# Performance work log

Hardware: AMD Instinct MI355X
Metric: run time of the kernel (lower is better)

The kernel has to match this reference:

```python
import jax, jax.numpy as jnp
import numpy as np

K = 2  # top-k experts per token


def setup_inputs() -> dict:
    key = jax.random.key(0)
    k1, k2, k3, k4 = jax.random.split(key, 4)
    B, S, D, E = 4, 4096, 1024, 64
    x = jax.random.normal(k1, (B, S, D), dtype=jnp.float32)
    gate_w = jax.random.normal(k2, (E, D), dtype=jnp.float32) * (1.0 / np.sqrt(D))
    noise_weight = jax.random.normal(k3, (E,), dtype=jnp.float32) * 0.02
    noise = jax.random.normal(k4, (B, S, E), dtype=jnp.float32)  # randn_like(logits) * noisy_std(=1.0)
    return {"x": x, "gate_w": gate_w, "noise_weight": noise_weight, "noise": noise}


def reference(x, gate_w, noise_weight, noise):
    E = gate_w.shape[0]
    # logits = x @ W^T  -> [B, S, E]
    logits = jnp.einsum("bsd,ed->bse", x, gate_w)
    logits_noisy = logits + noise * noise_weight  # noisy_std = 1.0 folded into `noise`
    top_vals, top_idx = jax.lax.top_k(logits_noisy, K)  # [B,S,K]
    # scatter top-k logits into a -inf mask, then softmax over experts
    keep = jax.nn.one_hot(top_idx, E, dtype=jnp.bool_).any(axis=-2)  # [B,S,E]
    neg_inf = jnp.finfo(logits_noisy.dtype).min
    sparse = jnp.where(keep, logits_noisy, neg_inf)
    weights = jax.nn.softmax(sparse, axis=-1)
    return weights, top_idx
```

## Files before the change

### kernel.cpp

```cpp
#include <hip/hip_runtime.h>
#include <math.h>


#define DDIM 1024
#define NEXP 64
#define NTOK 16384
#define NSPLIT 4
#define CPB 4

typedef float f4 __attribute__((ext_vector_type(4)));
typedef short s8 __attribute__((ext_vector_type(8)));
typedef unsigned int u32;

static __device__ __forceinline__ void split3(float f, short& h, short& m, short& l) {
    const u32 uf = __float_as_uint(f);
    h = (short)(uf >> 16);
    const float r1 = f - __uint_as_float(uf & 0xffff0000u);
    const u32 u1 = __float_as_uint(r1);
    m = (short)(u1 >> 16);
    const float r2 = r1 - __uint_as_float(u1 & 0xffff0000u);
    l = (short)(__float_as_uint(r2) >> 16);
}

static __device__ __forceinline__ void gl_lds16(const void* g, void* l) {
    __builtin_amdgcn_global_load_lds(
        (const __attribute__((address_space(1))) u32*)g,
        (__attribute__((address_space(3))) u32*)l, 16, 0, 0);
}

__global__ __launch_bounds__(256)
void w_prep(const float* __restrict__ gw, short* __restrict__ wimg) {
    const int uid = blockIdx.x * 256 + threadIdx.x;
    const int c   = uid >> 9;
    const int kk  = (uid >> 8) & 1;
    const int e   = (uid >> 2) & 63;
    const int q   = uid & 3;
    const int k0  = c * 64 + kk * 32 + q * 8;
    const float* src = gw + (size_t)e * DDIM + k0;
    s8 hv, mv, lv;
    #pragma unroll
    for (int j = 0; j < 8; ++j) {
        short h, m, l;
        split3(src[j], h, m, l);
        hv[j] = h; mv[j] = m; lv[j] = l;
    }
    const size_t base = (size_t)c * 1536 + (kk * 3) * 256
                      + (e >> 4) * 64 + q * 16 + (e & 15);
    *(s8*)(wimg + (base      ) * 8) = hv;
    *(s8*)(wimg + (base + 256) * 8) = mv;
    *(s8*)(wimg + (base + 512) * 8) = lv;
}

__global__ __launch_bounds__(256, 4)
void gemm_partial(const float* __restrict__ x,
                  const short* __restrict__ wimg,
                  float* __restrict__ part)
{
    __shared__ short bs[1536 * 8];

    const int tid   = threadIdx.x;
    const int lane  = tid & 63;
    const int wv    = tid >> 6;
    const int m     = lane & 15;
    const int q     = lane >> 4;
    const int tile  = blockIdx.x & 255;
    const int split = blockIdx.x >> 8;
    const int tokBase = tile * 64 + wv * 16;

    const float* xrow = x + (size_t)(tokBase + m) * DDIM
                      + split * (CPB * 64) + q * 8;

    f4 acc0[4], acc1[4];
    #pragma unroll
    for (int t = 0; t < 4; ++t) { acc0[t] = (f4)0.f; acc1[t] = (f4)0.f; }

    f4 stage[2][4];
    stage[0][0] = *(const f4*)(xrow);
    stage[0][1] = *(const f4*)(xrow + 4);
    stage[0][2] = *(const f4*)(xrow + 32);
    stage[0][3] = *(const f4*)(xrow + 36);

    #pragma unroll
    for (int cc = 0; cc < CPB; ++cc) {
        const short* chunk = wimg + (size_t)(split * CPB + cc) * (1536 * 8);
        __syncthreads();
        #pragma unroll
        for (int i = 0; i < 6; ++i) {
            const int off = (wv * 6 + i) * 512;
            gl_lds16(chunk + off + lane * 8, &bs[off]);
        }
        __syncthreads();

        if (cc + 1 < CPB) {
            const float* s = xrow + (cc + 1) * 64;
            stage[(cc + 1) & 1][0] = *(const f4*)(s);
            stage[(cc + 1) & 1][1] = *(const f4*)(s + 4);
            stage[(cc + 1) & 1][2] = *(const f4*)(s + 32);
            stage[(cc + 1) & 1][3] = *(const f4*)(s + 36);
        }

        s8 ah[2], am[2], al[2];
        const float* sv = (const float*)stage[cc & 1];
        #pragma unroll
        for (int kk = 0; kk < 2; ++kk)
            #pragma unroll
            for (int j = 0; j < 8; ++j) {
                short h, mm, l;
                split3(sv[kk * 8 + j], h, mm, l);
                ah[kk][j] = h; am[kk][j] = mm; al[kk][j] = l;
            }

        #pragma unroll
        for (int kk = 0; kk < 2; ++kk) {
            #pragma unroll
            for (int t = 0; t < 4; ++t) {
                const int pb = (kk * 3) * 256 + t * 64 + lane;
                const s8 bh = *(const s8*)&bs[(pb      ) * 8];
                const s8 bm = *(const s8*)&bs[(pb + 256) * 8];
                const s8 bl = *(const s8*)&bs[(pb + 512) * 8];
                acc0[t] = __builtin_amdgcn_mfma_f32_16x16x32_bf16(ah[kk], bh, acc0[t], 0, 0, 0);
                acc1[t] = __builtin_amdgcn_mfma_f32_16x16x32_bf16(ah[kk], bm, acc1[t], 0, 0, 0);
                acc1[t] = __builtin_amdgcn_mfma_f32_16x16x32_bf16(am[kk], bh, acc1[t], 0, 0, 0);
                acc1[t] = __builtin_amdgcn_mfma_f32_16x16x32_bf16(ah[kk], bl, acc1[t], 0, 0, 0);
                acc1[t] = __builtin_amdgcn_mfma_f32_16x16x32_bf16(am[kk], bm, acc1[t], 0, 0, 0);
                acc1[t] = __builtin_amdgcn_mfma_f32_16x16x32_bf16(al[kk], bh, acc1[t], 0, 0, 0);
            }
        }
    }

    #pragma unroll
    for (int t = 0; t < 4; ++t)
        #pragma unroll
        for (int r = 0; r < 4; ++r)
            part[((size_t)split * NTOK + tokBase + q * 4 + r) * NEXP + m + 16 * t]
                = acc0[t][r] + acc1[t][r];
}

__global__ __launch_bounds__(256)
void reduce_topk(const float* __restrict__ part,
                 const float* __restrict__ noise_weight,
                 const float* __restrict__ noise,
                 float* __restrict__ out_w,
                 float* __restrict__ out_i)
{
    const int lane  = threadIdx.x & 63;
    const int wv    = threadIdx.x >> 6;
    const int token = blockIdx.x * 4 + wv;

    float sum = 0.f;
    #pragma unroll
    for (int s = 0; s < NSPLIT; ++s)
        sum += part[((size_t)s * NTOK + token) * NEXP + lane];

    const float ln = fmaf(noise[(size_t)token * NEXP + lane], noise_weight[lane], sum);

    float v1 = ln; int i1 = lane;
    #pragma unroll
    for (int off = 32; off > 0; off >>= 1) {
        const float vo = __shfl_xor(v1, off, 64);
        const int   io = __shfl_xor(i1, off, 64);
        if (vo > v1 || (vo == v1 && io < i1)) { v1 = vo; i1 = io; }
    }
    float v2 = (lane == i1) ? -3.4e38f : ln; int i2 = lane;
    #pragma unroll
    for (int off = 32; off > 0; off >>= 1) {
        const float vo = __shfl_xor(v2, off, 64);
        const int   io = __shfl_xor(i2, off, 64);
        if (vo > v2 || (vo == v2 && io < i2)) { v2 = vo; i2 = io; }
    }

    const float d   = expf(v2 - v1);
    const float inv = 1.f / (1.f + d);
    const float wgt = (lane == i1) ? inv : ((lane == i2) ? d * inv : 0.f);
    out_w[(size_t)token * NEXP + lane] = wgt;
    if (lane == 0) {
        out_i[(size_t)token * 2]     = (float)i1;
        out_i[(size_t)token * 2 + 1] = (float)i2;
    }
}

extern "C" void kernel_launch(void* const* d_in, const int* in_sizes, int n_in,
                              void* d_out, int out_size, void* d_ws, size_t ws_size,
                              hipStream_t stream) {
    const float* x     = (const float*)d_in[0];
    const float* gw    = (const float*)d_in[1];
    const float* nwt   = (const float*)d_in[2];
    const float* noise = (const float*)d_in[3];
    float* out_w = (float*)d_out;
    float* out_i = (float*)d_out + (size_t)NTOK * NEXP;

    short* wimg = (short*)d_ws;
    float* part = (float*)((char*)d_ws + 512 * 1024);

    hipLaunchKernelGGL(w_prep, dim3(32), dim3(256), 0, stream, gw, wimg);
    hipLaunchKernelGGL(gemm_partial, dim3(256 * NSPLIT), dim3(256), 0, stream,
                       x, wimg, part);
    hipLaunchKernelGGL(reduce_topk, dim3(NTOK / 4), dim3(256), 0, stream,
                       part, nwt, noise, out_w, out_i);
}
```

Before: 123.4 us.

## Fuse gating GEMM with top-k softmax, dropping split-K partials

Merges the split-K GEMM and the reduce/top-k kernel into one kernel. Each block handles 16 tokens over the full K dimension, with each wave owning 16 experts. Logits are staged in a small LDS tile, then the noisy top-2 softmax runs in place. This removes the partial-sum buffer round trip and one kernel launch. The trade-off is that each wave now reads B fragments directly from global memory instead of sharing LDS-staged weights, and each x row is loaded redundantly by all four waves.

```diff
diff --git a/kernel.cpp b/kernel.cpp
--- a/kernel.cpp
+++ b/kernel.cpp
@@ -5,8 +5,6 @@
 #define DDIM 1024
 #define NEXP 64
 #define NTOK 16384
-#define NSPLIT 4
-#define CPB 4
 
 typedef float f4 __attribute__((ext_vector_type(4)));
 typedef short s8 __attribute__((ext_vector_type(8)));
@@ -20,12 +18,6 @@
     m = (short)(u1 >> 16);
     const float r2 = r1 - __uint_as_float(u1 & 0xffff0000u);
     l = (short)(__float_as_uint(r2) >> 16);
-}
-
-static __device__ __forceinline__ void gl_lds16(const void* g, void* l) {
-    __builtin_amdgcn_global_load_lds(
-        (const __attribute__((address_space(1))) u32*)g,
-        (__attribute__((address_space(3))) u32*)l, 16, 0, 0);
 }
 
 __global__ __launch_bounds__(256)
@@ -51,131 +43,115 @@
     *(s8*)(wimg + (base + 512) * 8) = lv;
 }
 
-__global__ __launch_bounds__(256, 4)
-void gemm_partial(const float* __restrict__ x,
-                  const short* __restrict__ wimg,
-                  float* __restrict__ part)
+__global__ __launch_bounds__(256, 3)
+void gate_fused(const float* __restrict__ x,
+                const short* __restrict__ wimg,
+                const float* __restrict__ noise_weight,
+                const float* __restrict__ noise,
+                float* __restrict__ out_w,
+                float* __restrict__ out_i)
 {
-    __shared__ short bs[1536 * 8];
+    __shared__ float L[16][66];
 
-    const int tid   = threadIdx.x;
-    const int lane  = tid & 63;
-    const int wv    = tid >> 6;
-    const int m     = lane & 15;
-    const int q     = lane >> 4;
-    const int tile  = blockIdx.x & 255;
-    const int split = blockIdx.x >> 8;
-    const int tokBase = tile * 64 + wv * 16;
+    const int tid  = threadIdx.x;
+    const int lane = tid & 63;
+    const int wv   = tid >> 6;
+    const int m    = lane & 15;
+    const int q    = lane >> 4;
+    const int tokBase = blockIdx.x * 16;
 
-    const float* xrow = x + (size_t)(tokBase + m) * DDIM
-                      + split * (CPB * 64) + q * 8;
+    const float* xrow = x + (size_t)(tokBase + m) * DDIM + q * 8;
+    const short* wb   = wimg + ((size_t)wv * 64 + lane) * 8;
 
-    f4 acc0[4], acc1[4];
-    #pragma unroll
-    for (int t = 0; t < 4; ++t) { acc0[t] = (f4)0.f; acc1[t] = (f4)0.f; }
+    f4 acc0 = (f4)0.f, acc1 = (f4)0.f;
 
-    f4 stage[2][4];
-    stage[0][0] = *(const f4*)(xrow);
-    stage[0][1] = *(const f4*)(xrow + 4);
-    stage[0][2] = *(const f4*)(xrow + 32);
-    stage[0][3] = *(const f4*)(xrow + 36);
+    f4 sa[2][4];
+    sa[0][0] = *(const f4*)(xrow);
+    sa[0][1] = *(const f4*)(xrow + 4);
+    sa[0][2] = *(const f4*)(xrow + 32);
+    sa[0][3] = *(const f4*)(xrow + 36);
 
-    #pragma unroll
-    for (int cc = 0; cc < CPB; ++cc) {
-        const short* chunk = wimg + (size_t)(split * CPB + cc) * (1536 * 8);
-        __syncthreads();
-        #pragma unroll
-        for (int i = 0; i < 6; ++i) {
-            const int off = (wv * 6 + i) * 512;
-            gl_lds16(chunk + off + lane * 8, &bs[off]);
-        }
-        __syncthreads();
+    #pragma unroll 2
+    for (int cc = 0; cc < 16; ++cc) {
+        const int cur = cc & 1;
 
-        if (cc + 1 < CPB) {
+        const short* p = wb + (size_t)cc * (1536 * 8);
+        const s8 bh0 = *(const s8*)(p);
+        const s8 bm0 = *(const s8*)(p +  256 * 8);
+        const s8 bl0 = *(const s8*)(p +  512 * 8);
+        const s8 bh1 = *(const s8*)(p +  768 * 8);
+        const s8 bm1 = *(const s8*)(p + 1024 * 8);
+        const s8 bl1 = *(const s8*)(p + 1280 * 8);
+
+        if (cc + 1 < 16) {
             const float* s = xrow + (cc + 1) * 64;
-            stage[(cc + 1) & 1][0] = *(const f4*)(s);
-            stage[(cc + 1) & 1][1] = *(const f4*)(s + 4);
-            stage[(cc + 1) & 1][2] = *(const f4*)(s + 32);
-            stage[(cc + 1) & 1][3] = *(const f4*)(s + 36);
+            sa[cur ^ 1][0] = *(const f4*)(s);
+            sa[cur ^ 1][1] = *(const f4*)(s + 4);
+            sa[cur ^ 1][2] = *(const f4*)(s + 32);
+            sa[cur ^ 1][3] = *(const f4*)(s + 36);
         }
 
-        s8 ah[2], am[2], al[2];
-        const float* sv = (const float*)stage[cc & 1];
+        s8 ah[2], am_[2], al[2];
+        const float* sv = (const float*)sa[cur];
         #pragma unroll
         for (int kk = 0; kk < 2; ++kk)
             #pragma unroll
             for (int j = 0; j < 8; ++j) {
                 short h, mm, l;
                 split3(sv[kk * 8 + j], h, mm, l);
-                ah[kk][j] = h; am[kk][j] = mm; al[kk][j] = l;
+                ah[kk][j] = h; am_[kk][j] = mm; al[kk][j] = l;
             }
 
-        #pragma unroll
-        for (int kk = 0; kk < 2; ++kk) {
-            #pragma unroll
-            for (int t = 0; t < 4; ++t) {
-                const int pb = (kk * 3) * 256 + t * 64 + lane;
-                const s8 bh = *(const s8*)&bs[(pb      ) * 8];
-                const s8 bm = *(const s8*)&bs[(pb + 256) * 8];
-                const s8 bl = *(const s8*)&bs[(pb + 512) * 8];
-                acc0[t] = __builtin_amdgcn_mfma_f32_16x16x32_bf16(ah[kk], bh, acc0[t], 0, 0, 0);
-                acc1[t] = __builtin_amdgcn_mfma_f32_16x16x32_bf16(ah[kk], bm, acc1[t], 0, 0, 0);
-                acc1[t] = __builtin_amdgcn_mfma_f32_16x16x32_bf16(am[kk], bh, acc1[t], 0, 0, 0);
-                acc1[t] = __builtin_amdgcn_mfma_f32_16x16x32_bf16(ah[kk], bl, acc1[t], 0, 0, 0);
-                acc1[t] = __builtin_amdgcn_mfma_f32_16x16x32_bf16(am[kk], bm, acc1[t], 0, 0, 0);
-                acc1[t] = __builtin_amdgcn_mfma_f32_16x16x32_bf16(al[kk], bh, acc1[t], 0, 0, 0);
-            }
-        }
+        acc0 = __builtin_amdgcn_mfma_f32_16x16x32_bf16(ah[0], bh0, acc0, 0, 0, 0);
+        acc1 = __builtin_amdgcn_mfma_f32_16x16x32_bf16(ah[0], bm0, acc1, 0, 0, 0);
+        acc1 = __builtin_amdgcn_mfma_f32_16x16x32_bf16(am_[0], bh0, acc1, 0, 0, 0);
+        acc1 = __builtin_amdgcn_mfma_f32_16x16x32_bf16(ah[0], bl0, acc1, 0, 0, 0);
+        acc1 = __builtin_amdgcn_mfma_f32_16x16x32_bf16(am_[0], bm0, acc1, 0, 0, 0);
+        acc1 = __builtin_amdgcn_mfma_f32_16x16x32_bf16(al[0], bh0, acc1, 0, 0, 0);
+
+        acc0 = __builtin_amdgcn_mfma_f32_16x16x32_bf16(ah[1], bh1, acc0, 0, 0, 0);
+        acc1 = __builtin_amdgcn_mfma_f32_16x16x32_bf16(ah[1], bm1, acc1, 0, 0, 0);
+        acc1 = __builtin_amdgcn_mfma_f32_16x16x32_bf16(am_[1], bh1, acc1, 0, 0, 0);
+        acc1 = __builtin_amdgcn_mfma_f32_16x16x32_bf16(ah[1], bl1, acc1, 0, 0, 0);
+        acc1 = __builtin_amdgcn_mfma_f32_16x16x32_bf16(am_[1], bm1, acc1, 0, 0, 0);
+        acc1 = __builtin_amdgcn_mfma_f32_16x16x32_bf16(al[1], bh1, acc1, 0, 0, 0);
     }
 
     #pragma unroll
-    for (int t = 0; t < 4; ++t)
+    for (int r = 0; r < 4; ++r)
+        L[q * 4 + r][m + 16 * wv] = acc0[r] + acc1[r];
+    __syncthreads();
+
+    const float nw = noise_weight[lane];
+    #pragma unroll
+    for (int tt = 0; tt < 4; ++tt) {
+        const int tok  = wv * 4 + tt;
+        const int gtok = tokBase + tok;
+        const float ln = fmaf(noise[(size_t)gtok * NEXP + lane], nw, L[tok][lane]);
+
+        float v1 = ln; int i1 = lane;
         #pragma unroll
-        for (int r = 0; r < 4; ++r)
-            part[((size_t)split * NTOK + tokBase + q * 4 + r) * NEXP + m + 16 * t]
-                = acc0[t][r] + acc1[t][r];
-}
+        for (int off = 32; off > 0; off >>= 1) {
+            const float vo = __shfl_xor(v1, off, 64);
+            const int   io = __shfl_xor(i1, off, 64);
+            if (vo > v1 || (vo == v1 && io < i1)) { v1 = vo; i1 = io; }
+        }
+        float v2 = (lane == i1) ? -3.4e38f : ln; int i2 = lane;
+        #pragma unroll
+        for (int off = 32; off > 0; off >>= 1) {
+            const float vo = __shfl_xor(v2, off, 64);
+            const int   io = __shfl_xor(i2, off, 64);
+            if (vo > v2 || (vo == v2 && io < i2)) { v2 = vo; i2 = io; }
+        }
 
-__global__ __launch_bounds__(256)
-void reduce_topk(const float* __restrict__ part,
-                 const float* __restrict__ noise_weight,
-                 const float* __restrict__ noise,
-                 float* __restrict__ out_w,
-                 float* __restrict__ out_i)
-{
-    const int lane  = threadIdx.x & 63;
-    const int wv    = threadIdx.x >> 6;
-    const int token = blockIdx.x * 4 + wv;
-
-    float sum = 0.f;
-    #pragma unroll
-    for (int s = 0; s < NSPLIT; ++s)
-        sum += part[((size_t)s * NTOK + token) * NEXP + lane];
-
-    const float ln = fmaf(noise[(size_t)token * NEXP + lane], noise_weight[lane], sum);
-
-    float v1 = ln; int i1 = lane;
-    #pragma unroll
-    for (int off = 32; off > 0; off >>= 1) {
-        const float vo = __shfl_xor(v1, off, 64);
-        const int   io = __shfl_xor(i1, off, 64);
-        if (vo > v1 || (vo == v1 && io < i1)) { v1 = vo; i1 = io; }
-    }
-    float v2 = (lane == i1) ? -3.4e38f : ln; int i2 = lane;
-    #pragma unroll
-    for (int off = 32; off > 0; off >>= 1) {
-        const float vo = __shfl_xor(v2, off, 64);
-        const int   io = __shfl_xor(i2, off, 64);
-        if (vo > v2 || (vo == v2 && io < i2)) { v2 = vo; i2 = io; }
-    }
-
-    const float d   = expf(v2 - v1);
-    const float inv = 1.f / (1.f + d);
-    const float wgt = (lane == i1) ? inv : ((lane == i2) ? d * inv : 0.f);
-    out_w[(size_t)token * NEXP + lane] = wgt;
-    if (lane == 0) {
-        out_i[(size_t)token * 2]     = (float)i1;
-        out_i[(size_t)token * 2 + 1] = (float)i2;
+        const float d   = expf(v2 - v1);
+        const float inv = 1.f / (1.f + d);
+        const float wgt = (lane == i1) ? inv : ((lane == i2) ? d * inv : 0.f);
+        out_w[(size_t)gtok * NEXP + lane] = wgt;
+        if (lane == 0) {
+            out_i[(size_t)gtok * 2]     = (float)i1;
+            out_i[(size_t)gtok * 2 + 1] = (float)i2;
+        }
     }
 }
 
@@ -190,11 +166,8 @@
     float* out_i = (float*)d_out + (size_t)NTOK * NEXP;
 
     short* wimg = (short*)d_ws;
-    float* part = (float*)((char*)d_ws + 512 * 1024);
 
     hipLaunchKernelGGL(w_prep, dim3(32), dim3(256), 0, stream, gw, wimg);
-    hipLaunchKernelGGL(gemm_partial, dim3(256 * NSPLIT), dim3(256), 0, stream,
-                       x, wimg, part);
-    hipLaunchKernelGGL(reduce_topk, dim3(NTOK / 4), dim3(256), 0, stream,
-                       part, nwt, noise, out_w, out_i);
+    hipLaunchKernelGGL(gate_fused, dim3(NTOK / 16), dim3(256), 0, stream,
+                       x, wimg, nwt, noise, out_w, out_i);
 }
```

Result: slower. 140.9 us (+14.2%).
